# Optimization experiments

Hardware: AMD Instinct MI355X
Metric: run time of the kernel (lower is better)

Reference implementation:

```python
import jax, jax.numpy as jnp
import numpy as np
from jax import lax

TAU = 0.5       # opt.tau
EPSILON = 1e-3  # opt.epsilon


def setup_inputs() -> dict:
    key = jax.random.key(0)
    k1, k2, k3, k4 = jax.random.split(key, 4)
    B, Cin, H, W = 32, 64, 64, 64
    Cout, KS = 256, 5
    x = jax.random.normal(k1, (B, Cin, H, W), dtype=jnp.float32)
    # W_ff: OIHW conv kernel (Kaiming-ish scale)
    W_ff = jax.random.normal(k2, (Cout, Cin, KS, KS), dtype=jnp.float32) * (1.0 / np.sqrt(Cin * KS * KS))
    # W_rec: 1x1 recurrent conv, stored as [out, out]; small so the LCA loop converges
    W_rec = jax.random.normal(k3, (Cout, Cout), dtype=jnp.float32) * 0.01
    threshold = 0.1 * jax.random.normal(k4, (Cout,), dtype=jnp.float32)
    return {"x": x, "W_ff": W_ff, "W_rec": W_rec, "threshold": threshold, "max_n_iter": 20}


def _fro(v):
    return jnp.linalg.norm(v.ravel())


def _forward(x, W_ff, W_rec, threshold, max_n_iter):
    max_iter = max_n_iter * int(1.0 / TAU)
    # u_0 = W_ff * input  (valid conv, no bias)  -> [B, Cout, Ho, Wo]
    u0 = lax.conv_general_dilated(x, W_ff, window_strides=(1, 1), padding='VALID',
                                  dimension_numbers=('NCHW', 'OIHW', 'NCHW'))
    thr = threshold[None, :, None, None]
    a0 = jax.nn.relu(u0 - thr)
    u_init = jnp.zeros_like(u0)

    def cond(state):
        _, _, i, converged = state
        return jnp.logical_and(jnp.logical_not(converged), i <= max_iter)

    def body(state):
        u, a, i, _ = state
        # 1x1 recurrent conv == channel matmul
        rec = jnp.einsum('oi,bixy->boxy', W_rec, a)
        u_new = (1.0 - TAU) * u + TAU * (u0 - rec)
        a_new = jax.nn.relu(u_new - thr)
        converged = (_fro(u_new - u) / _fro(u_new)) < EPSILON
        return (u_new, a_new, i + 1, converged)

    _, a_final, _, _ = lax.while_loop(cond, body, (u_init, a0, jnp.int32(0), jnp.array(False)))
    # original torch code detaches activities throughout the loop and at return
    return lax.stop_gradient(a_final)


def reference(x, W_ff, W_rec, threshold, max_n_iter):
    return _forward(x, W_ff, W_rec, threshold, max_n_iter)
```

## Files before the change

kernel.cpp:

```cpp
#include <hip/hip_runtime.h>


typedef __attribute__((ext_vector_type(8))) short short8;
typedef __attribute__((ext_vector_type(4))) float f32x4;

#define NTOT 115200
#define CHW  262144
#define HW2  4096
#define LDA  264
#define LDC  40

__device__ __forceinline__ unsigned short f2bf(float f) {
  unsigned int u = __float_as_uint(f);
  unsigned int r = u + 0x7FFFu + ((u >> 16) & 1u);
  return (unsigned short)(r >> 16);
}
__device__ __forceinline__ float bf2f(unsigned short h) {
  return __uint_as_float(((unsigned int)h) << 16);
}
__device__ __forceinline__ unsigned short f2h(float f) {
  _Float16 x = (_Float16)f;
  unsigned short r;
  __builtin_memcpy(&r, &x, 2);
  return r;
}
__device__ __forceinline__ float h2f(unsigned short h) {
  _Float16 x;
  __builtin_memcpy(&x, &h, 2);
  return (float)x;
}

__global__ void cast_weights(const float* __restrict__ wff_f,
                             const float* __restrict__ wrec_f,
                             unsigned short* __restrict__ wff,
                             unsigned short* __restrict__ wrec_sw) {
  int tid = blockIdx.x * 256 + threadIdx.x;
  if (tid < 409600) {
    int o = tid / 1600, k = tid % 1600;
    int kk = k >> 6, ci = k & 63;
    wff[tid] = f2bf(wff_f[o * 1600 + ci * 25 + kk]);
  } else if (tid < 409600 + 65536) {
    int i = tid - 409600;
    int o = i >> 8, ic = i & 255;
    wrec_sw[(((ic >> 3) << 8) + o) * 8 + (ic & 7)] = f2bf(wrec_f[i]);
  }
}

__global__ __launch_bounds__(256) void transpose_x(
    const float* __restrict__ x, unsigned short* __restrict__ xt) {
  int g = blockIdx.x * 256 + threadIdx.x;
  const float* src = x + (long)(g >> 12) * CHW + (g & 4095);
  unsigned short* dst = xt + (long)g * 64;
#pragma unroll
  for (int oct = 0; oct < 8; ++oct) {
    alignas(16) unsigned short tmp[8];
#pragma unroll
    for (int d = 0; d < 8; ++d)
      tmp[d] = f2bf(src[(oct * 8 + d) * HW2]);
    *(int4*)(dst + oct * 8) = *(const int4*)tmp;
  }
}

__global__ __launch_bounds__(256) void conv_kernel(
    const unsigned short* __restrict__ xt,
    const unsigned short* __restrict__ wff,
    unsigned short* __restrict__ u0_fl) {
  __shared__ short As[128 * LDC];
  __shared__ short Bs[128 * LDC];
  const int t = threadIdx.x;
  const int n0 = blockIdx.x * 128;
  const int oc0 = blockIdx.y * 128;
  const int lane = t & 63, w = t >> 6;
  const int q = lane >> 4, r = lane & 15;
  const int woc = w >> 1, wn = w & 1;
  const int qt = t & 3, mrow = t >> 2;

  int xbase[2];
#pragma unroll
  for (int p = 0; p < 2; ++p) {
    int n = n0 + p * 64 + mrow;
    int bb = n / 3600, rem = n - bb * 3600;
    int yy = rem / 60, xx = rem - yy * 60;
    xbase[p] = (bb * 4096 + yy * 64 + xx) * 64 + qt * 8;
  }

  f32x4 acc[4][4];
#pragma unroll
  for (int i = 0; i < 4; i++)
#pragma unroll
    for (int j = 0; j < 4; j++) acc[i][j] = (f32x4){0.f, 0.f, 0.f, 0.f};

  for (int c = 0; c < 50; ++c) {
    const int k0 = c * 32;
    const int kk = c >> 1;
    const int ky = kk / 5, kx = kk - ky * 5;
    const int choff = (ky * 64 + kx) * 64 + (c & 1) * 32;

    __syncthreads();
#pragma unroll
    for (int p = 0; p < 2; ++p) {
      int m = p * 64 + mrow;
      *(int4*)(&Bs[m * LDC + qt * 8]) =
          *(const int4*)(wff + (oc0 + m) * 1600 + k0 + qt * 8);
    }
#pragma unroll
    for (int p = 0; p < 2; ++p) {
      int m = p * 64 + mrow;
      *(int4*)(&As[m * LDC + qt * 8]) = *(const int4*)(xt + xbase[p] + choff);
    }
    __syncthreads();

    short8 xf[4], wf[4];
#pragma unroll
    for (int j = 0; j < 4; j++)
      xf[j] = *(const short8*)(&As[(wn * 64 + j * 16 + r) * LDC + q * 8]);
#pragma unroll
    for (int i = 0; i < 4; i++)
      wf[i] = *(const short8*)(&Bs[(woc * 64 + i * 16 + r) * LDC + q * 8]);
#pragma unroll
    for (int i = 0; i < 4; i++)
#pragma unroll
      for (int j = 0; j < 4; j++)
        acc[i][j] = __builtin_amdgcn_mfma_f32_16x16x32_bf16(wf[i], xf[j],
                                                            acc[i][j], 0, 0, 0);
  }

  const int tile = blockIdx.x * 2 + wn;
#pragma unroll
  for (int j = 0; j < 4; j++) {
#pragma unroll
    for (int p = 0; p < 2; p++) {
      const int w_fl = blockIdx.y * 4 + woc * 2 + p;
      alignas(16) unsigned short up[8];
#pragma unroll
      for (int d = 0; d < 4; ++d) up[d] = f2h(acc[2 * p][j][d]);
#pragma unroll
      for (int d = 0; d < 4; ++d) up[4 + d] = f2h(acc[2 * p + 1][j][d]);
      *(int4*)(&u0_fl[tile * 16384 + j * 4096 + (w_fl * 64 + q * 16 + r) * 8]) =
          *(const int4*)up;
    }
  }
}

__device__ __forceinline__ void gemm_acc8(const short* a_lds,
                                          const unsigned short* __restrict__
                                              wrec_sw,
                                          int w, int q, int r,
                                          f32x4 acc[2][4]) {
#pragma unroll
  for (int i = 0; i < 2; i++)
#pragma unroll
    for (int j = 0; j < 4; j++) acc[i][j] = (f32x4){0.f, 0.f, 0.f, 0.f};

#pragma unroll
  for (int c = 0; c < 8; ++c) {
    short8 afr[2], bfr[4];
#pragma unroll
    for (int i = 0; i < 2; i++)
      afr[i] = *(const short8*)(wrec_sw +
               (((c * 4 + q) << 8) + w * 32 + i * 16 + r) * 8);
#pragma unroll
    for (int j = 0; j < 4; j++)
      bfr[j] = *(const short8*)(&a_lds[(j * 16 + r) * LDA + c * 32 + q * 8]);
#pragma unroll
    for (int i = 0; i < 2; i++)
#pragma unroll
      for (int j = 0; j < 4; j++)
        acc[i][j] = __builtin_amdgcn_mfma_f32_16x16x32_bf16(afr[i], bfr[j],
                                                            acc[i][j], 0, 0, 0);
  }
}

template <int FIRST>
__global__ __launch_bounds__(512, 4) void iter_pair(
    const unsigned short* __restrict__ wrec_sw,
    const unsigned short* __restrict__ u0, const float* __restrict__ thr,
    const unsigned short* __restrict__ uin,
    unsigned short* __restrict__ uA, unsigned short* __restrict__ uB,
    float* __restrict__ norms, int* __restrict__ flag, int itA) {
  __shared__ short a_lds[64 * LDA];
  __shared__ float red[32];

  const int t = threadIdx.x;
  if (!FIRST) {
    if (*(volatile int*)flag) return;
    float dA = 0.f, nA = 0.f, dB = 0.f, nB = 0.f;
#pragma unroll
    for (int s = 0; s < 8; ++s) {
      dA += norms[(itA - 2) * 16 + s];
      nA += norms[(itA - 2) * 16 + 8 + s];
      dB += norms[(itA - 1) * 16 + s];
      nB += norms[(itA - 1) * 16 + 8 + s];
    }
    if (dA < 1e-6f * nA || dB < 1e-6f * nB) {
      if (t == 0) *flag = 1;
      return;
    }
  }

  const int lane = t & 63, w = t >> 6;
  const int q = lane >> 4, r = lane & 15;
  const unsigned base = blockIdx.x * 16384 + t * 8;

  float thc[2][4];
#pragma unroll
  for (int i = 0; i < 2; ++i) {
    float4 th = *(const float4*)(thr + w * 32 + i * 16 + q * 4);
    thc[i][0] = th.x; thc[i][1] = th.y; thc[i][2] = th.z; thc[i][3] = th.w;
  }

  int4 sv[4], u0c[4];
#pragma unroll
  for (int j = 0; j < 4; ++j) {
    u0c[j] = *(const int4*)(u0 + base + j * 4096);
    sv[j] = FIRST ? u0c[j] : *(const int4*)(uin + base + j * 4096);
  }

#pragma unroll
  for (int j = 0; j < 4; ++j) {
    const unsigned short* hs = (const unsigned short*)&sv[j];
#pragma unroll
    for (int i = 0; i < 2; ++i) {
      alignas(8) unsigned short ap[4];
#pragma unroll
      for (int d = 0; d < 4; ++d) {
        float a = h2f(hs[i * 4 + d]) - thc[i][d];
        ap[d] = f2bf(a > 0.f ? a : 0.f);
      }
      *(uint2*)(&a_lds[(j * 16 + r) * LDA + w * 32 + i * 16 + q * 4]) =
          *(const uint2*)ap;
    }
  }
  __syncthreads();

  f32x4 acc[2][4];
  gemm_acc8(a_lds, wrec_sw, w, q, r, acc);

  float d2A = 0.f, n2A = 0.f;
#pragma unroll
  for (int j = 0; j < 4; ++j) {
    const unsigned short* us = (const unsigned short*)&u0c[j];
    const unsigned short* hs = (const unsigned short*)&sv[j];
    alignas(16) unsigned short up[8];
#pragma unroll
    for (int i = 0; i < 2; ++i)
#pragma unroll
      for (int d = 0; d < 4; ++d) {
        float uo = FIRST ? 0.f : h2f(hs[i * 4 + d]);
        float un = 0.5f * uo + 0.5f * (h2f(us[i * 4 + d]) - acc[i][j][d]);
        float df = un - uo;
        d2A += df * df;
        n2A += un * un;
        up[i * 4 + d] = f2h(un);
      }
    sv[j] = *(const int4*)up;
    *(int4*)(uA + base + j * 4096) = sv[j];
  }
  __syncthreads();

#pragma unroll
  for (int j = 0; j < 4; ++j) {
    const unsigned short* hs = (const unsigned short*)&sv[j];
#pragma unroll
    for (int i = 0; i < 2; ++i) {
      alignas(8) unsigned short ap[4];
#pragma unroll
      for (int d = 0; d < 4; ++d) {
        float a = h2f(hs[i * 4 + d]) - thc[i][d];
        ap[d] = f2bf(a > 0.f ? a : 0.f);
      }
      *(uint2*)(&a_lds[(j * 16 + r) * LDA + w * 32 + i * 16 + q * 4]) =
          *(const uint2*)ap;
    }
  }
  __syncthreads();

  gemm_acc8(a_lds, wrec_sw, w, q, r, acc);

  float d2B = 0.f, n2B = 0.f;
#pragma unroll
  for (int j = 0; j < 4; ++j) {
    const unsigned short* us = (const unsigned short*)&u0c[j];
    const unsigned short* hs = (const unsigned short*)&sv[j];
    alignas(16) unsigned short up[8];
#pragma unroll
    for (int i = 0; i < 2; ++i)
#pragma unroll
      for (int d = 0; d < 4; ++d) {
        float uo = h2f(hs[i * 4 + d]);
        float un = 0.5f * uo + 0.5f * (h2f(us[i * 4 + d]) - acc[i][j][d]);
        float df = un - uo;
        d2B += df * df;
        n2B += un * un;
        up[i * 4 + d] = f2h(un);
      }
    *(int4*)(uB + base + j * 4096) = *(const int4*)up;
  }

#pragma unroll
  for (int off = 32; off; off >>= 1) {
    d2A += __shfl_down(d2A, off, 64);
    n2A += __shfl_down(n2A, off, 64);
    d2B += __shfl_down(d2B, off, 64);
    n2B += __shfl_down(n2B, off, 64);
  }
  if (lane == 0) {
    red[w] = d2A; red[8 + w] = n2A; red[16 + w] = d2B; red[24 + w] = n2B;
  }
  __syncthreads();
  if (t == 0) {
    float a0 = 0.f, a1 = 0.f, a2 = 0.f, a3 = 0.f;
#pragma unroll
    for (int s = 0; s < 8; ++s) {
      a0 += red[s]; a1 += red[8 + s]; a2 += red[16 + s]; a3 += red[24 + s];
    }
    const int slot = blockIdx.x & 7;
    atomicAdd(&norms[itA * 16 + slot], a0);
    atomicAdd(&norms[itA * 16 + 8 + slot], a1);
    atomicAdd(&norms[(itA + 1) * 16 + slot], a2);
    atomicAdd(&norms[(itA + 1) * 16 + 8 + slot], a3);
  }
}

template <int FIRST>
__global__ __launch_bounds__(512, 4) void iter_one(
    const unsigned short* __restrict__ wrec_sw,
    const unsigned short* __restrict__ u0, const float* __restrict__ thr,
    const unsigned short* __restrict__ uin, unsigned short* __restrict__ uout,
    float* __restrict__ norms, int* __restrict__ flag, int it) {
  __shared__ short a_lds[64 * LDA];
  __shared__ float red[16];

  const int t = threadIdx.x;
  if (!FIRST) {
    if (*(volatile int*)flag) return;
    float dA = 0.f, nA = 0.f, dB = 0.f, nB = 0.f;
#pragma unroll
    for (int s = 0; s < 8; ++s) {
      dA += norms[(it - 2) * 16 + s];
      nA += norms[(it - 2) * 16 + 8 + s];
      dB += norms[(it - 1) * 16 + s];
      nB += norms[(it - 1) * 16 + 8 + s];
    }
    if (dA < 1e-6f * nA || dB < 1e-6f * nB) {
      if (t == 0) *flag = 1;
      return;
    }
  }

  const int lane = t & 63, w = t >> 6;
  const int q = lane >> 4, r = lane & 15;
  const unsigned base = blockIdx.x * 16384 + t * 8;

  float thc[2][4];
#pragma unroll
  for (int i = 0; i < 2; ++i) {
    float4 th = *(const float4*)(thr + w * 32 + i * 16 + q * 4);
    thc[i][0] = th.x; thc[i][1] = th.y; thc[i][2] = th.z; thc[i][3] = th.w;
  }

  int4 sv[4], u0c[4];
#pragma unroll
  for (int j = 0; j < 4; ++j) {
    u0c[j] = *(const int4*)(u0 + base + j * 4096);
    sv[j] = FIRST ? u0c[j] : *(const int4*)(uin + base + j * 4096);
  }

#pragma unroll
  for (int j = 0; j < 4; ++j) {
    const unsigned short* hs = (const unsigned short*)&sv[j];
#pragma unroll
    for (int i = 0; i < 2; ++i) {
      alignas(8) unsigned short ap[4];
#pragma unroll
      for (int d = 0; d < 4; ++d) {
        float a = h2f(hs[i * 4 + d]) - thc[i][d];
        ap[d] = f2bf(a > 0.f ? a : 0.f);
      }
      *(uint2*)(&a_lds[(j * 16 + r) * LDA + w * 32 + i * 16 + q * 4]) =
          *(const uint2*)ap;
    }
  }
  __syncthreads();

  f32x4 acc[2][4];
  gemm_acc8(a_lds, wrec_sw, w, q, r, acc);

  float d2 = 0.f, n2 = 0.f;
#pragma unroll
  for (int j = 0; j < 4; ++j) {
    const unsigned short* us = (const unsigned short*)&u0c[j];
    const unsigned short* hs = (const unsigned short*)&sv[j];
    alignas(16) unsigned short up[8];
#pragma unroll
    for (int i = 0; i < 2; ++i)
#pragma unroll
      for (int d = 0; d < 4; ++d) {
        float uo = FIRST ? 0.f : h2f(hs[i * 4 + d]);
        float un = 0.5f * uo + 0.5f * (h2f(us[i * 4 + d]) - acc[i][j][d]);
        float df = un - uo;
        d2 += df * df;
        n2 += un * un;
        up[i * 4 + d] = f2h(un);
      }
    *(int4*)(uout + base + j * 4096) = *(const int4*)up;
  }

#pragma unroll
  for (int off = 32; off; off >>= 1) {
    d2 += __shfl_down(d2, off, 64);
    n2 += __shfl_down(n2, off, 64);
  }
  if (lane == 0) { red[w] = d2; red[8 + w] = n2; }
  __syncthreads();
  if (t == 0) {
    float a0 = 0.f, a1 = 0.f;
#pragma unroll
    for (int s = 0; s < 8; ++s) { a0 += red[s]; a1 += red[8 + s]; }
    const int slot = blockIdx.x & 7;
    atomicAdd(&norms[it * 16 + slot], a0);
    atomicAdd(&norms[it * 16 + 8 + slot], a1);
  }
}

__global__ void sel_kernel(const float* __restrict__ norms,
                           int* __restrict__ sel) {
  int it = 1;
  for (; it <= 41; ++it) {
    float d = 0.f, n = 0.f;
    for (int s = 0; s < 8; ++s) {
      d += norms[it * 16 + s];
      n += norms[it * 16 + 8 + s];
    }
    if (d < 1e-6f * n) break;
  }
  if (it > 41) it = 41;
  *sel = (it & 1) ? 0 : 1;
}
__global__ void set_sel(int* __restrict__ sel, int v) { *sel = v; }

__global__ __launch_bounds__(512) void final_out(
    const unsigned short* __restrict__ uA,
    const unsigned short* __restrict__ uB, const int* __restrict__ sel,
    const float* __restrict__ thr, float* __restrict__ out) {
  const unsigned short* u = (*sel) ? uB : uA;
  const int t = threadIdx.x;
  const int lane = t & 63, w = t >> 6;
  const int q = lane >> 4, r = lane & 15;
  const unsigned base = blockIdx.x * 16384 + t * 8;

  float thc[2][4];
#pragma unroll
  for (int i = 0; i < 2; ++i) {
    float4 th = *(const float4*)(thr + w * 32 + i * 16 + q * 4);
    thc[i][0] = th.x; thc[i][1] = th.y; thc[i][2] = th.z; thc[i][3] = th.w;
  }

#pragma unroll
  for (int j = 0; j < 4; ++j) {
    int4 raw = *(const int4*)(u + base + j * 4096);
    const unsigned short* rs = (const unsigned short*)&raw;
    const int n = blockIdx.x * 64 + j * 16 + r;
    const int b = n / 3600, s = n - b * 3600;
    float* ob = out + (long)b * 921600 + s;
#pragma unroll
    for (int i = 0; i < 2; ++i)
#pragma unroll
      for (int d = 0; d < 4; ++d) {
        const int oc = w * 32 + i * 16 + q * 4 + d;
        float v = h2f(rs[i * 4 + d]) - thc[i][d];
        ob[oc * 3600] = v > 0.f ? v : 0.f;
      }
  }
}

extern "C" void kernel_launch(void* const* d_in, const int* in_sizes, int n_in,
                              void* d_out, int out_size, void* d_ws,
                              size_t ws_size, hipStream_t stream) {
  const float* x      = (const float*)d_in[0];
  const float* wff_f  = (const float*)d_in[1];
  const float* wrec_f = (const float*)d_in[2];
  const float* thr    = (const float*)d_in[3];
  float* out = (float*)d_out;

  char* ws = (char*)d_ws;
  int* flag = (int*)ws;
  int* sel  = (int*)(ws + 8);
  float* norms = (float*)(ws + 64);
  unsigned short* wff     = (unsigned short*)(ws + 4096);
  unsigned short* wrec_sw = (unsigned short*)(ws + 823296);
  unsigned short* xt = (unsigned short*)(ws + 983040);
  unsigned short* uB = (unsigned short*)(ws + 983040);
  unsigned short* u0 = (unsigned short*)(ws + 59965440);
  unsigned short* uA = (unsigned short*)(ws + 118947840);
  const size_t NEEDED = 118947840ULL + 58982400ULL;

  hipMemsetAsync(d_ws, 0, 4096, stream);
  cast_weights<<<1856, 256, 0, stream>>>(wff_f, wrec_f, wff, wrec_sw);
  transpose_x<<<512, 256, 0, stream>>>(x, xt);
  conv_kernel<<<dim3(900, 2), 256, 0, stream>>>(xt, wff, u0);

  if (ws_size >= NEEDED) {
    iter_pair<1><<<1800, 512, 0, stream>>>(wrec_sw, u0, thr, uB, uA, uB,
                                           norms, flag, 1);
    for (int itA = 3; itA <= 39; itA += 2)
      iter_pair<0><<<1800, 512, 0, stream>>>(wrec_sw, u0, thr, uB, uA, uB,
                                             norms, flag, itA);
    iter_one<0><<<1800, 512, 0, stream>>>(wrec_sw, u0, thr, uB, uA, norms,
                                          flag, 41);
    sel_kernel<<<1, 1, 0, stream>>>(norms, sel);
  } else {
    iter_one<1><<<1800, 512, 0, stream>>>(wrec_sw, u0, thr, uB, uB, norms,
                                          flag, 1);
    for (int it = 2; it <= 41; ++it)
      iter_one<0><<<1800, 512, 0, stream>>>(wrec_sw, u0, thr, uB, uB, norms,
                                            flag, it);
    set_sel<<<1, 1, 0, stream>>>(sel, 1);
  }
  final_out<<<1800, 512, 0, stream>>>(uA, uB, sel, thr, out);
}
```

Measured before the change: 1.076 ms.

## Fuse LCA iterations into persistent cooperative kernel with register-resident state

Replaces the chain of per-iteration kernel launches with a single cooperative persistent kernel of 450 blocks. Each block keeps its u state for four tiles in registers as fp16, runs the recurrent GEMM step, reduces the convergence norms through atomics and a grid sync, and writes the final relu output directly. The aim is to remove about 40 kernel launches and the global-memory round trips of u per iteration. In exchange it depends on all 450 blocks being co-resident (falls back to the old path if the cooperative launch fails), may face register pressure from the large sv array, and adds a grid-wide barrier every iteration.

```diff
diff --git a/kernel.cpp b/kernel.cpp
--- a/kernel.cpp
+++ b/kernel.cpp
@@ -1,4 +1,7 @@
 #include <hip/hip_runtime.h>
+#include <hip/hip_cooperative_groups.h>
+
+namespace cg = cooperative_groups;
 
 
 typedef __attribute__((ext_vector_type(8))) short short8;
@@ -142,6 +145,162 @@
   }
 }
 
+__global__ __launch_bounds__(512, 4) void iter_persist(
+    const unsigned short* __restrict__ wrec_sw,
+    const unsigned short* __restrict__ u0,
+    const float* __restrict__ thr,
+    float* __restrict__ norms,
+    float* __restrict__ out) {
+  __shared__ short a_lds[64 * LDA];
+  __shared__ float red[16];
+
+  const int t = threadIdx.x;
+  const int lane = t & 63, w = t >> 6;
+  const int q = lane >> 4, r = lane & 15;
+
+  float thc[2][4];
+#pragma unroll
+  for (int i = 0; i < 2; ++i) {
+    float4 th = *(const float4*)(thr + w * 32 + i * 16 + q * 4);
+    thc[i][0] = th.x; thc[i][1] = th.y; thc[i][2] = th.z; thc[i][3] = th.w;
+  }
+
+  cg::grid_group grid = cg::this_grid();
+
+  int4 sv[4][4];
+#pragma unroll
+  for (int tt = 0; tt < 4; ++tt) {
+    const unsigned base = (blockIdx.x * 4 + tt) * 16384 + t * 8;
+#pragma unroll
+    for (int j = 0; j < 4; ++j)
+      sv[tt][j] = *(const int4*)(u0 + base + j * 4096);
+  }
+
+  int it = 1;
+  for (;; ++it) {
+    float d2 = 0.f, n2 = 0.f;
+#pragma unroll
+    for (int tt = 0; tt < 4; ++tt) {
+      const unsigned base = (blockIdx.x * 4 + tt) * 16384 + t * 8;
+#pragma unroll
+      for (int j = 0; j < 4; ++j) {
+        const unsigned short* hs = (const unsigned short*)&sv[tt][j];
+#pragma unroll
+        for (int i = 0; i < 2; ++i) {
+          alignas(8) unsigned short ap[4];
+#pragma unroll
+          for (int d = 0; d < 4; ++d) {
+            float a = h2f(hs[i * 4 + d]) - thc[i][d];
+            ap[d] = f2bf(a > 0.f ? a : 0.f);
+          }
+          *(uint2*)(&a_lds[(j * 16 + r) * LDA + w * 32 + i * 16 + q * 4]) =
+              *(const uint2*)ap;
+        }
+      }
+      __syncthreads();
+
+#pragma unroll
+      for (int h = 0; h < 2; ++h) {
+        int4 u0h[2];
+#pragma unroll
+        for (int jj = 0; jj < 2; ++jj)
+          u0h[jj] = *(const int4*)(u0 + base + (h * 2 + jj) * 4096);
+
+        f32x4 acc[2][2];
+#pragma unroll
+        for (int i = 0; i < 2; i++)
+#pragma unroll
+          for (int jj = 0; jj < 2; jj++) acc[i][jj] = (f32x4){0.f, 0.f, 0.f, 0.f};
+#pragma unroll
+        for (int c = 0; c < 8; ++c) {
+          short8 afr[2];
+#pragma unroll
+          for (int i = 0; i < 2; i++)
+            afr[i] = *(const short8*)(wrec_sw +
+                     (((c * 4 + q) << 8) + w * 32 + i * 16 + r) * 8);
+#pragma unroll
+          for (int jj = 0; jj < 2; ++jj) {
+            short8 bfr = *(const short8*)(
+                &a_lds[((h * 2 + jj) * 16 + r) * LDA + c * 32 + q * 8]);
+#pragma unroll
+            for (int i = 0; i < 2; i++)
+              acc[i][jj] = __builtin_amdgcn_mfma_f32_16x16x32_bf16(
+                  afr[i], bfr, acc[i][jj], 0, 0, 0);
+          }
+        }
+
+#pragma unroll
+        for (int jj = 0; jj < 2; ++jj) {
+          const int j = h * 2 + jj;
+          const unsigned short* us = (const unsigned short*)&u0h[jj];
+          const unsigned short* hs = (const unsigned short*)&sv[tt][j];
+          alignas(16) unsigned short up[8];
+#pragma unroll
+          for (int i = 0; i < 2; ++i)
+#pragma unroll
+            for (int d = 0; d < 4; ++d) {
+              float uo = (it == 1) ? 0.f : h2f(hs[i * 4 + d]);
+              float un = 0.5f * uo +
+                         0.5f * (h2f(us[i * 4 + d]) - acc[i][jj][d]);
+              float df = un - uo;
+              d2 += df * df;
+              n2 += un * un;
+              up[i * 4 + d] = f2h(un);
+            }
+          sv[tt][j] = *(const int4*)up;
+        }
+      }
+      __syncthreads();
+    }
+
+#pragma unroll
+    for (int off = 32; off; off >>= 1) {
+      d2 += __shfl_down(d2, off, 64);
+      n2 += __shfl_down(n2, off, 64);
+    }
+    if (lane == 0) { red[w] = d2; red[8 + w] = n2; }
+    __syncthreads();
+    if (t == 0) {
+      float a0 = 0.f, a1 = 0.f;
+#pragma unroll
+      for (int s = 0; s < 8; ++s) { a0 += red[s]; a1 += red[8 + s]; }
+      const int slot = blockIdx.x & 7;
+      atomicAdd(&norms[it * 16 + slot], a0);
+      atomicAdd(&norms[it * 16 + 8 + slot], a1);
+    }
+    grid.sync();
+    float ds = 0.f, ns = 0.f;
+#pragma unroll
+    for (int s = 0; s < 8; ++s) {
+      ds += __hip_atomic_load(&norms[it * 16 + s], __ATOMIC_RELAXED,
+                              __HIP_MEMORY_SCOPE_AGENT);
+      ns += __hip_atomic_load(&norms[it * 16 + 8 + s], __ATOMIC_RELAXED,
+                              __HIP_MEMORY_SCOPE_AGENT);
+    }
+    if (ds < 1e-6f * ns || it == 41) break;
+  }
+
+#pragma unroll
+  for (int tt = 0; tt < 4; ++tt) {
+    const int tile = blockIdx.x * 4 + tt;
+#pragma unroll
+    for (int j = 0; j < 4; ++j) {
+      const int n = tile * 64 + j * 16 + r;
+      const int b = n / 3600, s = n - b * 3600;
+      float* ob = out + (long)b * 921600 + s;
+      const unsigned short* hs = (const unsigned short*)&sv[tt][j];
+#pragma unroll
+      for (int i = 0; i < 2; ++i)
+#pragma unroll
+        for (int d = 0; d < 4; ++d) {
+          const int oc = w * 32 + i * 16 + q * 4 + d;
+          float v = h2f(hs[i * 4 + d]) - thc[i][d];
+          ob[oc * 3600] = v > 0.f ? v : 0.f;
+        }
+    }
+  }
+}
+
 __device__ __forceinline__ void gemm_acc8(const short* a_lds,
                                           const unsigned short* __restrict__
                                               wrec_sw,
@@ -500,22 +659,34 @@
   transpose_x<<<512, 256, 0, stream>>>(x, xt);
   conv_kernel<<<dim3(900, 2), 256, 0, stream>>>(xt, wff, u0);
 
-  if (ws_size >= NEEDED) {
-    iter_pair<1><<<1800, 512, 0, stream>>>(wrec_sw, u0, thr, uB, uA, uB,
-                                           norms, flag, 1);
-    for (int itA = 3; itA <= 39; itA += 2)
-      iter_pair<0><<<1800, 512, 0, stream>>>(wrec_sw, u0, thr, uB, uA, uB,
-                                             norms, flag, itA);
-    iter_one<0><<<1800, 512, 0, stream>>>(wrec_sw, u0, thr, uB, uA, norms,
-                                          flag, 41);
-    sel_kernel<<<1, 1, 0, stream>>>(norms, sel);
-  } else {
-    iter_one<1><<<1800, 512, 0, stream>>>(wrec_sw, u0, thr, uB, uB, norms,
-                                          flag, 1);
-    for (int it = 2; it <= 41; ++it)
-      iter_one<0><<<1800, 512, 0, stream>>>(wrec_sw, u0, thr, uB, uB, norms,
-                                            flag, it);
-    set_sel<<<1, 1, 0, stream>>>(sel, 1);
-  }
-  final_out<<<1800, 512, 0, stream>>>(uA, uB, sel, thr, out);
-}
+  const unsigned short* p_wrec = wrec_sw;
+  const unsigned short* p_u0 = u0;
+  const float* p_thr = thr;
+  float* p_norms = norms;
+  float* p_out = out;
+  void* cargs[] = {(void*)&p_wrec, (void*)&p_u0, (void*)&p_thr,
+                   (void*)&p_norms, (void*)&p_out};
+  hipError_t rc = hipLaunchCooperativeKernel(
+      (const void*)iter_persist, dim3(450), dim3(512), cargs, 0, stream);
+
+  if (rc != hipSuccess) {
+    if (ws_size >= NEEDED) {
+      iter_pair<1><<<1800, 512, 0, stream>>>(wrec_sw, u0, thr, uB, uA, uB,
+                                             norms, flag, 1);
+      for (int itA = 3; itA <= 39; itA += 2)
+        iter_pair<0><<<1800, 512, 0, stream>>>(wrec_sw, u0, thr, uB, uA, uB,
+                                               norms, flag, itA);
+      iter_one<0><<<1800, 512, 0, stream>>>(wrec_sw, u0, thr, uB, uA, norms,
+                                            flag, 41);
+      sel_kernel<<<1, 1, 0, stream>>>(norms, sel);
+    } else {
+      iter_one<1><<<1800, 512, 0, stream>>>(wrec_sw, u0, thr, uB, uB, norms,
+                                            flag, 1);
+      for (int it = 2; it <= 41; ++it)
+        iter_one<0><<<1800, 512, 0, stream>>>(wrec_sw, u0, thr, uB, uB, norms,
+                                              flag, it);
+      set_sel<<<1, 1, 0, stream>>>(sel, 1);
+    }
+    final_out<<<1800, 512, 0, stream>>>(uA, uB, sel, thr, out);
+  }
+}
```

Result: slower. 2.987 ms (+177.7%).

## Fuse four LCA iterations per kernel launch and merge selection into output

Applied to the files above, without the earlier changes.

Adds an iter_quad kernel that runs four recurrent iterations per launch, keeping each block's u tile in registers across them and writing each iterate to one of four rotating buffers. This cuts the number of launches and the global re-reads of u between iterations. It also merges the single-thread select kernel into the final output kernel. In exchange it needs more workspace, and the convergence check becomes coarser: up to three extra iterations may run before an early exit is detected, and the stored buffers are used to pick the correct result.

```diff
diff --git a/kernel.cpp b/kernel.cpp
--- a/kernel.cpp
+++ b/kernel.cpp
@@ -172,6 +172,137 @@
 }
 
 template <int FIRST>
+__global__ __launch_bounds__(512, 4) void iter_quad(
+    const unsigned short* __restrict__ wrec_sw,
+    const unsigned short* __restrict__ u0, const float* __restrict__ thr,
+    const unsigned short* __restrict__ uin,
+    unsigned short* __restrict__ o1, unsigned short* __restrict__ o2,
+    unsigned short* __restrict__ o3, unsigned short* __restrict__ o4,
+    float* __restrict__ norms, int* __restrict__ flag, int it1) {
+  __shared__ short a_lds[64 * LDA];
+  __shared__ float red[64];
+
+  const int t = threadIdx.x;
+  if (!FIRST) {
+    if (*(volatile int*)flag) return;
+    bool hit = false;
+#pragma unroll
+    for (int rr = 0; rr < 4; ++rr) {
+      float d = 0.f, n = 0.f;
+#pragma unroll
+      for (int s = 0; s < 8; ++s) {
+        d += norms[(it1 - 4 + rr) * 16 + s];
+        n += norms[(it1 - 4 + rr) * 16 + 8 + s];
+      }
+      hit = hit || (d < 1e-6f * n);
+    }
+    if (hit) {
+      if (t == 0) *flag = 1;
+      return;
+    }
+  }
+
+  const int lane = t & 63, w = t >> 6;
+  const int q = lane >> 4, r = lane & 15;
+  const unsigned base = blockIdx.x * 16384 + t * 8;
+
+  float thc[2][4];
+#pragma unroll
+  for (int i = 0; i < 2; ++i) {
+    float4 th = *(const float4*)(thr + w * 32 + i * 16 + q * 4);
+    thc[i][0] = th.x; thc[i][1] = th.y; thc[i][2] = th.z; thc[i][3] = th.w;
+  }
+
+  int4 sv[4], u0c[4];
+#pragma unroll
+  for (int j = 0; j < 4; ++j) {
+    u0c[j] = *(const int4*)(u0 + base + j * 4096);
+    sv[j] = FIRST ? u0c[j] : *(const int4*)(uin + base + j * 4096);
+  }
+
+  float d2[4], n2[4];
+#pragma unroll
+  for (int p = 0; p < 4; ++p) { d2[p] = 0.f; n2[p] = 0.f; }
+
+#define QPHASE(PH, OUT)                                                       \
+  {                                                                           \
+    _Pragma("unroll")                                                         \
+    for (int j = 0; j < 4; ++j) {                                             \
+      const unsigned short* hs = (const unsigned short*)&sv[j];               \
+      _Pragma("unroll")                                                       \
+      for (int i = 0; i < 2; ++i) {                                           \
+        alignas(8) unsigned short ap[4];                                      \
+        _Pragma("unroll")                                                     \
+        for (int d = 0; d < 4; ++d) {                                         \
+          float a = h2f(hs[i * 4 + d]) - thc[i][d];                           \
+          ap[d] = f2bf(a > 0.f ? a : 0.f);                                    \
+        }                                                                     \
+        *(uint2*)(&a_lds[(j * 16 + r) * LDA + w * 32 + i * 16 + q * 4]) =     \
+            *(const uint2*)ap;                                                \
+      }                                                                       \
+    }                                                                         \
+    __syncthreads();                                                          \
+    f32x4 acc[2][4];                                                          \
+    gemm_acc8(a_lds, wrec_sw, w, q, r, acc);                                  \
+    _Pragma("unroll")                                                         \
+    for (int j = 0; j < 4; ++j) {                                             \
+      const unsigned short* us = (const unsigned short*)&u0c[j];              \
+      const unsigned short* hs = (const unsigned short*)&sv[j];               \
+      alignas(16) unsigned short up[8];                                       \
+      _Pragma("unroll")                                                       \
+      for (int i = 0; i < 2; ++i)                                             \
+        _Pragma("unroll")                                                     \
+        for (int d = 0; d < 4; ++d) {                                         \
+          float uo = (FIRST && (PH) == 1) ? 0.f : h2f(hs[i * 4 + d]);         \
+          float un = 0.5f * uo + 0.5f * (h2f(us[i * 4 + d]) - acc[i][j][d]);  \
+          float df = un - uo;                                                 \
+          d2[(PH)-1] += df * df;                                              \
+          n2[(PH)-1] += un * un;                                              \
+          up[i * 4 + d] = f2h(un);                                            \
+        }                                                                     \
+      sv[j] = *(const int4*)up;                                               \
+      *(int4*)((OUT) + base + j * 4096) = sv[j];                              \
+    }                                                                         \
+    __syncthreads();                                                          \
+  }
+
+  QPHASE(1, o1)
+  QPHASE(2, o2)
+  QPHASE(3, o3)
+  QPHASE(4, o4)
+#undef QPHASE
+
+#pragma unroll
+  for (int off = 32; off; off >>= 1)
+#pragma unroll
+    for (int p = 0; p < 4; ++p) {
+      d2[p] += __shfl_down(d2[p], off, 64);
+      n2[p] += __shfl_down(n2[p], off, 64);
+    }
+  if (lane == 0)
+#pragma unroll
+    for (int p = 0; p < 4; ++p) {
+      red[p * 16 + w] = d2[p];
+      red[p * 16 + 8 + w] = n2[p];
+    }
+  __syncthreads();
+  if (t == 0) {
+    const int slot = blockIdx.x & 7;
+#pragma unroll
+    for (int p = 0; p < 4; ++p) {
+      float a0 = 0.f, a1 = 0.f;
+#pragma unroll
+      for (int s = 0; s < 8; ++s) {
+        a0 += red[p * 16 + s];
+        a1 += red[p * 16 + 8 + s];
+      }
+      atomicAdd(&norms[(it1 + p) * 16 + slot], a0);
+      atomicAdd(&norms[(it1 + p) * 16 + 8 + slot], a1);
+    }
+  }
+}
+
+template <int FIRST>
 __global__ __launch_bounds__(512, 4) void iter_pair(
     const unsigned short* __restrict__ wrec_sw,
     const unsigned short* __restrict__ u0, const float* __restrict__ thr,
@@ -322,7 +453,7 @@
   }
 }
 
-template <int FIRST>
+template <int FIRST, int ROWS>
 __global__ __launch_bounds__(512, 4) void iter_one(
     const unsigned short* __restrict__ wrec_sw,
     const unsigned short* __restrict__ u0, const float* __restrict__ thr,
@@ -334,15 +465,18 @@
   const int t = threadIdx.x;
   if (!FIRST) {
     if (*(volatile int*)flag) return;
-    float dA = 0.f, nA = 0.f, dB = 0.f, nB = 0.f;
-#pragma unroll
-    for (int s = 0; s < 8; ++s) {
-      dA += norms[(it - 2) * 16 + s];
-      nA += norms[(it - 2) * 16 + 8 + s];
-      dB += norms[(it - 1) * 16 + s];
-      nB += norms[(it - 1) * 16 + 8 + s];
-    }
-    if (dA < 1e-6f * nA || dB < 1e-6f * nB) {
+    bool hit = false;
+#pragma unroll
+    for (int rr = 0; rr < ROWS; ++rr) {
+      float d = 0.f, n = 0.f;
+#pragma unroll
+      for (int s = 0; s < 8; ++s) {
+        d += norms[(it - ROWS + rr) * 16 + s];
+        n += norms[(it - ROWS + rr) * 16 + 8 + s];
+      }
+      hit = hit || (d < 1e-6f * n);
+    }
+    if (hit) {
       if (t == 0) *flag = 1;
       return;
     }
@@ -423,8 +557,11 @@
   }
 }
 
-__global__ void sel_kernel(const float* __restrict__ norms,
-                           int* __restrict__ sel) {
+__global__ __launch_bounds__(512) void final_sel(
+    const unsigned short* __restrict__ b0, const unsigned short* __restrict__ b1,
+    const unsigned short* __restrict__ b2, const unsigned short* __restrict__ b3,
+    const float* __restrict__ norms, const float* __restrict__ thr,
+    float* __restrict__ out) {
   int it = 1;
   for (; it <= 41; ++it) {
     float d = 0.f, n = 0.f;
@@ -435,15 +572,10 @@
     if (d < 1e-6f * n) break;
   }
   if (it > 41) it = 41;
-  *sel = (it & 1) ? 0 : 1;
-}
-__global__ void set_sel(int* __restrict__ sel, int v) { *sel = v; }
-
-__global__ __launch_bounds__(512) void final_out(
-    const unsigned short* __restrict__ uA,
-    const unsigned short* __restrict__ uB, const int* __restrict__ sel,
-    const float* __restrict__ thr, float* __restrict__ out) {
-  const unsigned short* u = (*sel) ? uB : uA;
+  const int k = (it - 1) & 3;
+  const unsigned short* u = (k & 2) ? ((k & 1) ? b3 : b2)
+                                    : ((k & 1) ? b1 : b0);
+
   const int t = threadIdx.x;
   const int lane = t & 63, w = t >> 6;
   const int q = lane >> 4, r = lane & 15;
@@ -485,37 +617,47 @@
 
   char* ws = (char*)d_ws;
   int* flag = (int*)ws;
-  int* sel  = (int*)(ws + 8);
   float* norms = (float*)(ws + 64);
   unsigned short* wff     = (unsigned short*)(ws + 4096);
   unsigned short* wrec_sw = (unsigned short*)(ws + 823296);
   unsigned short* xt = (unsigned short*)(ws + 983040);
-  unsigned short* uB = (unsigned short*)(ws + 983040);
+  unsigned short* uD = (unsigned short*)(ws + 983040);
   unsigned short* u0 = (unsigned short*)(ws + 59965440);
   unsigned short* uA = (unsigned short*)(ws + 118947840);
-  const size_t NEEDED = 118947840ULL + 58982400ULL;
+  unsigned short* uB = (unsigned short*)(ws + 177930240);
+  unsigned short* uC = (unsigned short*)(ws + 236912640);
+  const size_t NEED_QUAD = 236912640ULL + 58982400ULL;
+  const size_t NEED_PAIR = 118947840ULL + 58982400ULL;
 
   hipMemsetAsync(d_ws, 0, 4096, stream);
   cast_weights<<<1856, 256, 0, stream>>>(wff_f, wrec_f, wff, wrec_sw);
   transpose_x<<<512, 256, 0, stream>>>(x, xt);
   conv_kernel<<<dim3(900, 2), 256, 0, stream>>>(xt, wff, u0);
 
-  if (ws_size >= NEEDED) {
-    iter_pair<1><<<1800, 512, 0, stream>>>(wrec_sw, u0, thr, uB, uA, uB,
+  if (ws_size >= NEED_QUAD) {
+    iter_quad<1><<<1800, 512, 0, stream>>>(wrec_sw, u0, thr, uD, uA, uB, uC,
+                                           uD, norms, flag, 1);
+    for (int it1 = 5; it1 <= 37; it1 += 4)
+      iter_quad<0><<<1800, 512, 0, stream>>>(wrec_sw, u0, thr, uD, uA, uB, uC,
+                                             uD, norms, flag, it1);
+    iter_one<0, 4><<<1800, 512, 0, stream>>>(wrec_sw, u0, thr, uD, uA, norms,
+                                             flag, 41);
+    final_sel<<<1800, 512, 0, stream>>>(uA, uB, uC, uD, norms, thr, out);
+  } else if (ws_size >= NEED_PAIR) {
+    iter_pair<1><<<1800, 512, 0, stream>>>(wrec_sw, u0, thr, uD, uA, uD,
                                            norms, flag, 1);
     for (int itA = 3; itA <= 39; itA += 2)
-      iter_pair<0><<<1800, 512, 0, stream>>>(wrec_sw, u0, thr, uB, uA, uB,
+      iter_pair<0><<<1800, 512, 0, stream>>>(wrec_sw, u0, thr, uD, uA, uD,
                                              norms, flag, itA);
-    iter_one<0><<<1800, 512, 0, stream>>>(wrec_sw, u0, thr, uB, uA, norms,
-                                          flag, 41);
-    sel_kernel<<<1, 1, 0, stream>>>(norms, sel);
+    iter_one<0, 2><<<1800, 512, 0, stream>>>(wrec_sw, u0, thr, uD, uA, norms,
+                                             flag, 41);
+    final_sel<<<1800, 512, 0, stream>>>(uA, uD, uA, uD, norms, thr, out);
   } else {
-    iter_one<1><<<1800, 512, 0, stream>>>(wrec_sw, u0, thr, uB, uB, norms,
-                                          flag, 1);
+    iter_one<1, 0><<<1800, 512, 0, stream>>>(wrec_sw, u0, thr, uD, uD, norms,
+                                             flag, 1);
     for (int it = 2; it <= 41; ++it)
-      iter_one<0><<<1800, 512, 0, stream>>>(wrec_sw, u0, thr, uB, uB, norms,
-                                            flag, it);
-    set_sel<<<1, 1, 0, stream>>>(sel, 1);
-  }
-  final_out<<<1800, 512, 0, stream>>>(uA, uB, sel, thr, out);
-}
+      iter_one<0, 2><<<1800, 512, 0, stream>>>(wrec_sw, u0, thr, uD, uD,
+                                               norms, flag, it);
+    final_sel<<<1800, 512, 0, stream>>>(uD, uD, uD, uD, norms, thr, out);
+  }
+}
```

After: 991.1 us. 7.9% less time.
